# Performance work log

Hardware: AMD Instinct MI355X
Metric: run time of the kernel (lower is better)

The kernel has to match this reference:

```python
import jax, jax.numpy as jnp
import numpy as np

N, IN_FEAT, OUT_FEAT, H = 4096, 256, 256, 8
D = OUT_FEAT // H  # per-head dim = 32
ADJ_DENSITY = 0.05


def setup_inputs() -> dict:
    key = jax.random.key(0)
    kx, kw, kb, ka, kadj = jax.random.split(key, 5)
    x = jax.random.normal(kx, (N, IN_FEAT), dtype=jnp.float32)
    # eqx.nn.Linear params: weight [out, in], bias [out]
    W = jax.random.normal(kw, (OUT_FEAT, IN_FEAT), dtype=jnp.float32) * (1.0 / np.sqrt(IN_FEAT))
    b = jax.random.normal(kb, (OUT_FEAT,), dtype=jnp.float32) * 0.01
    a = jax.random.normal(ka, (H, 2 * D), dtype=jnp.float32)
    adj_matrix = jax.random.bernoulli(kadj, ADJ_DENSITY, (N, N)).astype(jnp.float32)
    return {"x": x, "W": W, "b": b, "a": a, "adj_matrix": adj_matrix}


def reference(x, W, b, a, adj_matrix):
    num_nodes = x.shape[0]
    num_heads = a.shape[0]
    half = a.shape[1] // 2
    # projection: [N, H*D] -> [N, H, D]
    node_feats = (x @ W.T + b).reshape(num_nodes, num_heads, half)
    # per-head additive attention halves -> [N, H]
    logit_parent = (node_feats * a[None, :, :half]).sum(axis=-1)
    logit_child = (node_feats * a[None, :, half:]).sum(axis=-1)
    # [N, N, H] dense logits via broadcast-add
    attn_logits = logit_parent[:, None, :] + logit_child[None, :, :]
    attn_logits = jax.nn.leaky_relu(attn_logits, 0.2)
    # NOTE: faithful to source — masked entries set to 0.0 (not -inf)
    attn_logits = jnp.where(jnp.abs(adj_matrix)[..., None] != 0.0, attn_logits, 0.0)
    attn_probs = jax.nn.softmax(attn_logits, axis=1)
    out = jnp.einsum('ijh,jhc->ihc', attn_probs, node_feats)
    return out.reshape(num_nodes, -1)
```

## Files before the change

kernel.cpp:

```cpp
#include <hip/hip_runtime.h>

#define NN    4096
#define OF    256
#define NH    8
#define MAXNZ 384

typedef __attribute__((ext_vector_type(8))) short short8;
typedef __attribute__((ext_vector_type(4))) float f32x4;

__device__ __forceinline__ float bf2f(unsigned int u) {
    union { unsigned int i; float f; } v; v.i = u << 16; return v.f;
}
__device__ __forceinline__ unsigned short f2bf(float f) {
    union { float f; unsigned int i; } v; v.f = f;
    unsigned int x = v.i;
    return (unsigned short)((x + 0x7fffu + ((x >> 16) & 1u)) >> 16);
}
__device__ __forceinline__ unsigned int pk2bf(float a, float b) {
    return (unsigned int)f2bf(a) | ((unsigned int)f2bf(b) << 16);
}

__global__ __launch_bounds__(256) void k_pre(
    const float* __restrict__ adjf, const float* __restrict__ Wf,
    int* __restrict__ flag, unsigned short* __restrict__ Wbh,
    unsigned short* __restrict__ Wbl, float* __restrict__ zbase)
{
    __shared__ int viol;
    int t = threadIdx.x;
    int gid = blockIdx.x * 256 + t;
    if (t == 0) viol = 0;
    __syncthreads();
    int bad = 0;
    for (int k = t; k < NN; k += 256) {
        float v = adjf[k];
        if (!(v == 0.0f || v == 1.0f)) bad = 1;
    }
    if (bad) atomicAdd(&viol, 1);
    __syncthreads();
    int f = viol > 0;
    if (t == 0) *flag = f;

    zbase[gid] = 0.f;
    if (gid < 256) zbase[65536 + gid] = 0.f;
    if (!f) {
        float v = Wf[gid];
        unsigned short h = f2bf(v);
        Wbh[gid] = h; Wbl[gid] = f2bf(v - bf2f(h));
    }
}

__global__ __launch_bounds__(256) void k_proj(
    const void* __restrict__ xraw, const void* __restrict__ Wraw,
    const void* __restrict__ braw, const void* __restrict__ araw,
    const int* __restrict__ flag,
    const unsigned short* __restrict__ Wbh, const unsigned short* __restrict__ Wbl,
    unsigned short* __restrict__ nfb, float* __restrict__ lp,
    float* __restrict__ lc, float* __restrict__ Stot)
{
    __shared__ unsigned short xh[16][264], xl[16][264];

    int f = *flag;
    int t = threadIdx.x;
    int wave = t >> 6;
    int lane = t & 63;
    int pid = blockIdx.x;

    int tid  = pid * 4 + wave;
    int mt = tid >> 4, nt = tid & 15;
    int lr = lane & 15;
    int kq = (lane >> 4) * 8;

    if (!f) {
        const float* xsrc = (const float*)xraw + (size_t)mt * 4096;
        #pragma unroll
        for (int q = 0; q < 16; q++) {
            int e = t + 256*q;
            float v = xsrc[e];
            unsigned short h = f2bf(v);
            xh[e >> 8][e & 255] = h;
            xl[e >> 8][e & 255] = f2bf(v - bf2f(h));
        }
        __syncthreads();
    }

    size_t wo = (size_t)(nt*16 + lr)*OF + kq;
    f32x4 acc = {0.f, 0.f, 0.f, 0.f};
    if (f) {
        const short8* xp = reinterpret_cast<const short8*>(
            (const unsigned short*)xraw + (size_t)(mt*16 + lr)*OF + kq);
        const short8* wp = reinterpret_cast<const short8*>(
            (const unsigned short*)Wraw + wo);
        #pragma unroll
        for (int kk = 0; kk < OF/32; kk++)
            acc = __builtin_amdgcn_mfma_f32_16x16x32_bf16(xp[kk*4], wp[kk*4], acc, 0, 0, 0);
    } else {
        const short8* wh = reinterpret_cast<const short8*>(Wbh + wo);
        const short8* wl = reinterpret_cast<const short8*>(Wbl + wo);
        #pragma unroll
        for (int kk = 0; kk < OF/32; kk++) {
            short8 ah = *reinterpret_cast<const short8*>(&xh[lr][kk*32 + kq]);
            short8 al = *reinterpret_cast<const short8*>(&xl[lr][kk*32 + kq]);
            short8 bh = wh[kk*4], bl = wl[kk*4];
            acc = __builtin_amdgcn_mfma_f32_16x16x32_bf16(ah, bh, acc, 0, 0, 0);
            acc = __builtin_amdgcn_mfma_f32_16x16x32_bf16(ah, bl, acc, 0, 0, 0);
            acc = __builtin_amdgcn_mfma_f32_16x16x32_bf16(al, bh, acc, 0, 0, 0);
        }
    }

    int col  = nt*16 + lr;
    int row0 = mt*16 + (lane >> 4) * 4;
    int h = col >> 5, cc = col & 31;
    float bias, apar, achd;
    if (f) {
        bias = bf2f((unsigned int)((const unsigned short*)braw)[col]);
        apar = bf2f((unsigned int)((const unsigned short*)araw)[h*64 + cc]);
        achd = bf2f((unsigned int)((const unsigned short*)araw)[h*64 + 32 + cc]);
    } else {
        bias = ((const float*)braw)[col];
        apar = ((const float*)araw)[h*64 + cc];
        achd = ((const float*)araw)[h*64 + 32 + cc];
    }
    float st = 0.f, pr[4], cr[4];
    #pragma unroll
    for (int r = 0; r < 4; r++) {
        float v = acc[r] + bias;
        nfb[(size_t)(row0 + r) * OF + col] = f2bf(v);
        st += v;
        pr[r] = v * apar;
        cr[r] = v * achd;
    }
    #pragma unroll
    for (int m = 1; m <= 8; m <<= 1) {
        #pragma unroll
        for (int r = 0; r < 4; r++) {
            pr[r] += __shfl_xor(pr[r], m, 64);
            cr[r] += __shfl_xor(cr[r], m, 64);
        }
    }
    if ((lane & 15) == 0) {
        #pragma unroll
        for (int r = 0; r < 4; r++) {
            atomicAdd(&lp[(row0 + r) * NH + h], pr[r]);
            atomicAdd(&lc[(row0 + r) * NH + h], cr[r]);
        }
    }
    st += __shfl_down(st, 16, 64);
    st += __shfl_down(st, 32, 64);
    if (lane < 16) atomicAdd(&Stot[col], st);
}

__global__ __launch_bounds__(256, 8) void k_attn(
    const int* __restrict__ flag, const float* __restrict__ adjf,
    const float* __restrict__ lp, const float* __restrict__ lc,
    const unsigned short* __restrict__ nfb, const float* __restrict__ Stot,
    void* __restrict__ outv)
{
    __shared__ int   jro[MAXNZ];
    __shared__ float zred[256];
    __shared__ float gred[3][256];
    __shared__ int   wtot[4];

    int i = blockIdx.x;
    int t = threadIdx.x;
    int lane = t & 63, wid = t >> 6;
    int f = *flag;
    int hh = lane >> 3;
    int slot = lane & 7;
    float lph = lp[i*NH + hh];

    unsigned int m16 = 0;
    if (f) {
        const uint4* ap = reinterpret_cast<const uint4*>(
            (const unsigned short*)adjf + (size_t)i * NN + wid * 1024);
        #pragma unroll
        for (int g = 0; g < 2; g++) {
            uint4 v = ap[lane + 64*g];
            unsigned int wd[4] = {v.x, v.y, v.z, v.w};
            #pragma unroll
            for (int u = 0; u < 4; u++) {
                if (wd[u] & 0xffffu) m16 |= 1u << (g*8 + 2*u);
                if (wd[u] >> 16)     m16 |= 1u << (g*8 + 2*u + 1);
            }
        }
    } else {
        const uint4* ap = reinterpret_cast<const uint4*>(
            adjf + (size_t)i * NN + wid * 1024);
        #pragma unroll
        for (int g = 0; g < 4; g++) {
            uint4 v = ap[lane + 64*g];
            if (v.x) m16 |= 1u << (g*4);
            if (v.y) m16 |= 1u << (g*4 + 1);
            if (v.z) m16 |= 1u << (g*4 + 2);
            if (v.w) m16 |= 1u << (g*4 + 3);
        }
    }

    int pc = __popc(m16);
    int pref = pc;
    #pragma unroll
    for (int off = 1; off < 64; off <<= 1) {
        int u = __shfl_up(pref, off, 64);
        if (lane >= off) pref += u;
    }
    if (lane == 63) wtot[wid] = pref;
    __syncthreads();
    int w0 = wtot[0], w1 = wtot[1], w2 = wtot[2], w3 = wtot[3];
    int n = min(w0 + w1 + w2 + w3, MAXNZ);
    int base = (wid > 0 ? w0 : 0) + (wid > 1 ? w1 : 0) + (wid > 2 ? w2 : 0);
    int pos = base + pref - pc;
    unsigned int mm = m16;
    int jb = wid * 1024;
    while (mm && pos < MAXNZ) {
        int q = __builtin_ctz(mm);
        mm &= mm - 1;
        int j = f ? (jb + lane*8 + ((q >> 3) << 9) + (q & 7))
                  : (jb + lane*4 + ((q >> 2) << 8) + (q & 3));
        jro[pos++] = j * OF;
    }
    __syncthreads();

    int c4 = lane * 4;
    float a0 = 0.f, a1 = 0.f, a2 = 0.f, a3 = 0.f;
    float zp = 0.f;
    int k = wid;
    for (; k + 28 < n; k += 32) {
        int jm = jro[k + 4*slot];
        float s = lph + lc[(jm >> 5) + hh];
        s = fmaxf(s, 0.2f * s);
        float wv = __expf(fminf(s, 70.f)) - 1.f;
        zp += wv;

        int jj[8]; uint2 d[8];
        #pragma unroll
        for (int u = 0; u < 8; u++) {
            jj[u] = __builtin_amdgcn_readfirstlane(jro[k + 4*u]);
            d[u] = *reinterpret_cast<const uint2*>(nfb + jj[u] + c4);
        }
        #pragma unroll
        for (int u = 0; u < 8; u++) {
            float w = __shfl(wv, (lane & ~7) | u, 64);
            a0 += w * bf2f(d[u].x & 0xffffu);
            a1 += w * bf2f(d[u].x >> 16);
            a2 += w * bf2f(d[u].y & 0xffffu);
            a3 += w * bf2f(d[u].y >> 16);
        }
    }
    for (; k < n; k += 4) {
        int j = __builtin_amdgcn_readfirstlane(jro[k]);
        float lcv = lc[(j >> 5) + hh];
        uint2 d = *reinterpret_cast<const uint2*>(nfb + j + c4);
        float s = lph + lcv;
        s = fmaxf(s, 0.2f * s);
        float w = __expf(fminf(s, 70.f)) - 1.f;
        if (slot == 0) zp += w;
        a0 += w * bf2f(d.x & 0xffffu);
        a1 += w * bf2f(d.x >> 16);
        a2 += w * bf2f(d.y & 0xffffu);
        a3 += w * bf2f(d.y >> 16);
    }
    zp += __shfl_xor(zp, 1, 64);
    zp += __shfl_xor(zp, 2, 64);
    zp += __shfl_xor(zp, 4, 64);
    zred[t] = zp;
    if (wid) {
        gred[wid-1][c4]   = a0; gred[wid-1][c4+1] = a1;
        gred[wid-1][c4+2] = a2; gred[wid-1][c4+3] = a3;
    }
    __syncthreads();

    if (wid == 0) {
        float z = zred[hh*8] + zred[64 + hh*8] + zred[128 + hh*8] + zred[192 + hh*8];
        float iz = 1.0f / (4096.0f + z);
        a0 += gred[0][c4]   + gred[1][c4]   + gred[2][c4];
        a1 += gred[0][c4+1] + gred[1][c4+1] + gred[2][c4+1];
        a2 += gred[0][c4+2] + gred[1][c4+2] + gred[2][c4+2];
        a3 += gred[0][c4+3] + gred[1][c4+3] + gred[2][c4+3];
        float4 stv = *reinterpret_cast<const float4*>(Stot + c4);
        float o0 = (stv.x + a0) * iz;
        float o1 = (stv.y + a1) * iz;
        float o2 = (stv.z + a2) * iz;
        float o3 = (stv.w + a3) * iz;
        if (f) {
            uint2 pk; pk.x = pk2bf(o0, o1); pk.y = pk2bf(o2, o3);
            *reinterpret_cast<uint2*>((unsigned short*)outv + (size_t)i*OF + c4) = pk;
        } else {
            float4 o = {o0, o1, o2, o3};
            *reinterpret_cast<float4*>((float*)outv + (size_t)i*OF + c4) = o;
        }
    }
}

extern "C" void kernel_launch(void* const* d_in, const int* in_sizes, int n_in,
                              void* d_out, int out_size, void* d_ws, size_t ws_size,
                              hipStream_t stream) {
    const void* x   = d_in[0];
    const void* W   = d_in[1];
    const void* b   = d_in[2];
    const void* a   = d_in[3];
    const void* adj = d_in[4];

    char* ws = (char*)d_ws;
    const size_t MB = 1024u*1024u, KB = 1024u;
    unsigned short* nfb  = (unsigned short*)(ws);
    float*          lp   = (float*)(ws + 2*MB);
    float*          lc   = (float*)(ws + 2*MB + 128*KB);
    float*          Stot = (float*)(ws + 2*MB + 256*KB);
    int*            flag = (int*)(ws + 2*MB + 257*KB);
    unsigned short* Wbh  = (unsigned short*)(ws + 6*MB);
    unsigned short* Wbl  = (unsigned short*)(ws + 6*MB + 128*KB);

    k_pre  <<<256,  256, 0, stream>>>((const float*)adj, (const float*)W,
                                      flag, Wbh, Wbl, lp);
    k_proj <<<1024, 256, 0, stream>>>(x, W, b, a, flag, Wbh, Wbl,
                                      nfb, lp, lc, Stot);
    k_attn <<<NN,   256, 0, stream>>>(flag, (const float*)adj, lp, lc,
                                      nfb, Stot, d_out);
}
```

Before: 156.6 us.

## Replace sparse gather attention with dense MFMA over transposed node features

The attention kernel no longer compacts nonzero adjacency entries and gathers rows. Each block now takes 16 rows and sweeps all 4096 columns densely. It builds masked exp weights in bf16 and multiplies them with transposed node features using MFMA. The projection kernel writes node features transposed, stores lc head-major and folds log2e into the logits so exp2 can be used. This removes the serial compaction and the irregular gathers, but it does dense work over an adjacency that is about 5% full and rounds the weights to bf16.

```diff
diff --git a/kernel.cpp b/kernel.cpp
--- a/kernel.cpp
+++ b/kernel.cpp
@@ -3,7 +3,6 @@
 #define NN    4096
 #define OF    256
 #define NH    8
-#define MAXNZ 384
 
 typedef __attribute__((ext_vector_type(8))) short short8;
 typedef __attribute__((ext_vector_type(4))) float f32x4;
@@ -18,6 +17,9 @@
 }
 __device__ __forceinline__ unsigned int pk2bf(float a, float b) {
     return (unsigned int)f2bf(a) | ((unsigned int)f2bf(b) << 16);
+}
+__device__ __forceinline__ float asf(unsigned int u) {
+    union { unsigned int i; float f; } v; v.i = u; return v.f;
 }
 
 __global__ __launch_bounds__(256) void k_pre(
@@ -54,7 +56,7 @@
     const void* __restrict__ braw, const void* __restrict__ araw,
     const int* __restrict__ flag,
     const unsigned short* __restrict__ Wbh, const unsigned short* __restrict__ Wbl,
-    unsigned short* __restrict__ nfb, float* __restrict__ lp,
+    unsigned short* __restrict__ nfT, float* __restrict__ lp,
     float* __restrict__ lc, float* __restrict__ Stot)
 {
     __shared__ unsigned short xh[16][264], xl[16][264];
@@ -110,6 +112,7 @@
     int col  = nt*16 + lr;
     int row0 = mt*16 + (lane >> 4) * 4;
     int h = col >> 5, cc = col & 31;
+    const float LOG2E = 1.4426950408889634f;
     float bias, apar, achd;
     if (f) {
         bias = bf2f((unsigned int)((const unsigned short*)braw)[col]);
@@ -120,14 +123,23 @@
         apar = ((const float*)araw)[h*64 + cc];
         achd = ((const float*)araw)[h*64 + 32 + cc];
     }
+    apar *= LOG2E; achd *= LOG2E;
+
+    float vv[4];
+    #pragma unroll
+    for (int r = 0; r < 4; r++) vv[r] = acc[r] + bias;
+
+    uint2 pkv;
+    pkv.x = pk2bf(vv[0], vv[1]);
+    pkv.y = pk2bf(vv[2], vv[3]);
+    *reinterpret_cast<uint2*>(nfT + (size_t)col*NN + row0) = pkv;
+
     float st = 0.f, pr[4], cr[4];
     #pragma unroll
     for (int r = 0; r < 4; r++) {
-        float v = acc[r] + bias;
-        nfb[(size_t)(row0 + r) * OF + col] = f2bf(v);
-        st += v;
-        pr[r] = v * apar;
-        cr[r] = v * achd;
+        st += vv[r];
+        pr[r] = vv[r] * apar;
+        cr[r] = vv[r] * achd;
     }
     #pragma unroll
     for (int m = 1; m <= 8; m <<= 1) {
@@ -141,7 +153,7 @@
         #pragma unroll
         for (int r = 0; r < 4; r++) {
             atomicAdd(&lp[(row0 + r) * NH + h], pr[r]);
-            atomicAdd(&lc[(row0 + r) * NH + h], cr[r]);
+            atomicAdd(&lc[(size_t)h * NN + row0 + r], cr[r]);
         }
     }
     st += __shfl_down(st, 16, 64);
@@ -149,143 +161,96 @@
     if (lane < 16) atomicAdd(&Stot[col], st);
 }
 
-__global__ __launch_bounds__(256, 8) void k_attn(
+__global__ __launch_bounds__(512) void k_attn(
     const int* __restrict__ flag, const float* __restrict__ adjf,
     const float* __restrict__ lp, const float* __restrict__ lc,
-    const unsigned short* __restrict__ nfb, const float* __restrict__ Stot,
+    const unsigned short* __restrict__ nfT, const float* __restrict__ Stot,
     void* __restrict__ outv)
 {
-    __shared__ int   jro[MAXNZ];
-    __shared__ float zred[256];
-    __shared__ float gred[3][256];
-    __shared__ int   wtot[4];
-
-    int i = blockIdx.x;
+    __shared__ float zsh[8][16];
+
+    int i0 = blockIdx.x * 16;
     int t = threadIdx.x;
-    int lane = t & 63, wid = t >> 6;
+    int w = t >> 6;
+    int lane = t & 63;
+    int r = lane & 15;
+    int q = lane >> 4;
     int f = *flag;
-    int hh = lane >> 3;
-    int slot = lane & 7;
-    float lph = lp[i*NH + hh];
-
-    unsigned int m16 = 0;
-    if (f) {
-        const uint4* ap = reinterpret_cast<const uint4*>(
-            (const unsigned short*)adjf + (size_t)i * NN + wid * 1024);
-        #pragma unroll
-        for (int g = 0; g < 2; g++) {
-            uint4 v = ap[lane + 64*g];
-            unsigned int wd[4] = {v.x, v.y, v.z, v.w};
+
+    float lpr = lp[(i0 + r) * NH + w];
+    const float* lcr = lc + (size_t)w * NN;
+    const unsigned short* b0p = nfT + (size_t)(w*32      + r) * NN;
+    const unsigned short* b1p = nfT + (size_t)(w*32 + 16 + r) * NN;
+
+    f32x4 acc0 = {0.f,0.f,0.f,0.f}, acc1 = {0.f,0.f,0.f,0.f};
+    float zacc = 0.f;
+
+    for (int j0 = 0; j0 < NN; j0 += 32) {
+        int jq = j0 + q*8;
+        short8 B0 = *reinterpret_cast<const short8*>(b0p + jq);
+        short8 B1 = *reinterpret_cast<const short8*>(b1p + jq);
+        float4 lca = *reinterpret_cast<const float4*>(lcr + jq);
+        float4 lcb = *reinterpret_cast<const float4*>(lcr + jq + 4);
+        float lv[8] = {lca.x, lca.y, lca.z, lca.w, lcb.x, lcb.y, lcb.z, lcb.w};
+        float mk[8];
+        if (f) {
+            uint4 av = *reinterpret_cast<const uint4*>(
+                (const unsigned short*)adjf + (size_t)(i0 + r) * NN + jq);
+            unsigned int wd[4] = {av.x, av.y, av.z, av.w};
             #pragma unroll
             for (int u = 0; u < 4; u++) {
-                if (wd[u] & 0xffffu) m16 |= 1u << (g*8 + 2*u);
-                if (wd[u] >> 16)     m16 |= 1u << (g*8 + 2*u + 1);
+                mk[2*u]   = bf2f(wd[u] & 0xffffu);
+                mk[2*u+1] = bf2f(wd[u] >> 16);
             }
-        }
-    } else {
-        const uint4* ap = reinterpret_cast<const uint4*>(
-            adjf + (size_t)i * NN + wid * 1024);
-        #pragma unroll
-        for (int g = 0; g < 4; g++) {
-            uint4 v = ap[lane + 64*g];
-            if (v.x) m16 |= 1u << (g*4);
-            if (v.y) m16 |= 1u << (g*4 + 1);
-            if (v.z) m16 |= 1u << (g*4 + 2);
-            if (v.w) m16 |= 1u << (g*4 + 3);
-        }
-    }
-
-    int pc = __popc(m16);
-    int pref = pc;
-    #pragma unroll
-    for (int off = 1; off < 64; off <<= 1) {
-        int u = __shfl_up(pref, off, 64);
-        if (lane >= off) pref += u;
-    }
-    if (lane == 63) wtot[wid] = pref;
+        } else {
+            float4 a0 = *reinterpret_cast<const float4*>(
+                adjf + (size_t)(i0 + r) * NN + jq);
+            float4 a1 = *reinterpret_cast<const float4*>(
+                adjf + (size_t)(i0 + r) * NN + jq + 4);
+            mk[0]=a0.x; mk[1]=a0.y; mk[2]=a0.z; mk[3]=a0.w;
+            mk[4]=a1.x; mk[5]=a1.y; mk[6]=a1.z; mk[7]=a1.w;
+        }
+        float wv[8];
+        #pragma unroll
+        for (int e = 0; e < 8; e++) {
+            float s = lpr + lv[e];
+            s = fmaxf(s, 0.2f * s);
+            s = fminf(s, 101.0f);
+            wv[e] = (exp2f(s) - 1.0f) * mk[e];
+        }
+        union { unsigned int u[4]; short8 s8; } A;
+        #pragma unroll
+        for (int p = 0; p < 4; p++) {
+            unsigned int pk;
+            asm("v_cvt_pk_bf16_f32 %0, %1, %2" : "=v"(pk)
+                : "v"(wv[2*p]), "v"(wv[2*p+1]));
+            A.u[p] = pk;
+            zacc += asf(pk << 16) + asf(pk & 0xffff0000u);
+        }
+        acc0 = __builtin_amdgcn_mfma_f32_16x16x32_bf16(A.s8, B0, acc0, 0, 0, 0);
+        acc1 = __builtin_amdgcn_mfma_f32_16x16x32_bf16(A.s8, B1, acc1, 0, 0, 0);
+    }
+
+    zacc += __shfl_xor(zacc, 16, 64);
+    zacc += __shfl_xor(zacc, 32, 64);
+    if (lane < 16) zsh[w][lane] = zacc;
     __syncthreads();
-    int w0 = wtot[0], w1 = wtot[1], w2 = wtot[2], w3 = wtot[3];
-    int n = min(w0 + w1 + w2 + w3, MAXNZ);
-    int base = (wid > 0 ? w0 : 0) + (wid > 1 ? w1 : 0) + (wid > 2 ? w2 : 0);
-    int pos = base + pref - pc;
-    unsigned int mm = m16;
-    int jb = wid * 1024;
-    while (mm && pos < MAXNZ) {
-        int q = __builtin_ctz(mm);
-        mm &= mm - 1;
-        int j = f ? (jb + lane*8 + ((q >> 3) << 9) + (q & 7))
-                  : (jb + lane*4 + ((q >> 2) << 8) + (q & 3));
-        jro[pos++] = j * OF;
-    }
-    __syncthreads();
-
-    int c4 = lane * 4;
-    float a0 = 0.f, a1 = 0.f, a2 = 0.f, a3 = 0.f;
-    float zp = 0.f;
-    int k = wid;
-    for (; k + 28 < n; k += 32) {
-        int jm = jro[k + 4*slot];
-        float s = lph + lc[(jm >> 5) + hh];
-        s = fmaxf(s, 0.2f * s);
-        float wv = __expf(fminf(s, 70.f)) - 1.f;
-        zp += wv;
-
-        int jj[8]; uint2 d[8];
-        #pragma unroll
-        for (int u = 0; u < 8; u++) {
-            jj[u] = __builtin_amdgcn_readfirstlane(jro[k + 4*u]);
-            d[u] = *reinterpret_cast<const uint2*>(nfb + jj[u] + c4);
-        }
-        #pragma unroll
-        for (int u = 0; u < 8; u++) {
-            float w = __shfl(wv, (lane & ~7) | u, 64);
-            a0 += w * bf2f(d[u].x & 0xffffu);
-            a1 += w * bf2f(d[u].x >> 16);
-            a2 += w * bf2f(d[u].y & 0xffffu);
-            a3 += w * bf2f(d[u].y >> 16);
-        }
-    }
-    for (; k < n; k += 4) {
-        int j = __builtin_amdgcn_readfirstlane(jro[k]);
-        float lcv = lc[(j >> 5) + hh];
-        uint2 d = *reinterpret_cast<const uint2*>(nfb + j + c4);
-        float s = lph + lcv;
-        s = fmaxf(s, 0.2f * s);
-        float w = __expf(fminf(s, 70.f)) - 1.f;
-        if (slot == 0) zp += w;
-        a0 += w * bf2f(d.x & 0xffffu);
-        a1 += w * bf2f(d.x >> 16);
-        a2 += w * bf2f(d.y & 0xffffu);
-        a3 += w * bf2f(d.y >> 16);
-    }
-    zp += __shfl_xor(zp, 1, 64);
-    zp += __shfl_xor(zp, 2, 64);
-    zp += __shfl_xor(zp, 4, 64);
-    zred[t] = zp;
-    if (wid) {
-        gred[wid-1][c4]   = a0; gred[wid-1][c4+1] = a1;
-        gred[wid-1][c4+2] = a2; gred[wid-1][c4+3] = a3;
-    }
-    __syncthreads();
-
-    if (wid == 0) {
-        float z = zred[hh*8] + zred[64 + hh*8] + zred[128 + hh*8] + zred[192 + hh*8];
-        float iz = 1.0f / (4096.0f + z);
-        a0 += gred[0][c4]   + gred[1][c4]   + gred[2][c4];
-        a1 += gred[0][c4+1] + gred[1][c4+1] + gred[2][c4+1];
-        a2 += gred[0][c4+2] + gred[1][c4+2] + gred[2][c4+2];
-        a3 += gred[0][c4+3] + gred[1][c4+3] + gred[2][c4+3];
-        float4 stv = *reinterpret_cast<const float4*>(Stot + c4);
-        float o0 = (stv.x + a0) * iz;
-        float o1 = (stv.y + a1) * iz;
-        float o2 = (stv.z + a2) * iz;
-        float o3 = (stv.w + a3) * iz;
+
+    f32x4 z4 = *reinterpret_cast<f32x4*>(&zsh[w][q*4]);
+    int c0 = w*32 + r, c1 = c0 + 16;
+    float st0 = Stot[c0], st1 = Stot[c1];
+    #pragma unroll
+    for (int reg = 0; reg < 4; reg++) {
+        float iz = 1.0f / (4096.0f + z4[reg]);
+        float o0 = (st0 + acc0[reg]) * iz;
+        float o1 = (st1 + acc1[reg]) * iz;
+        int row = i0 + 4*q + reg;
         if (f) {
-            uint2 pk; pk.x = pk2bf(o0, o1); pk.y = pk2bf(o2, o3);
-            *reinterpret_cast<uint2*>((unsigned short*)outv + (size_t)i*OF + c4) = pk;
+            ((unsigned short*)outv)[(size_t)row*OF + c0] = f2bf(o0);
+            ((unsigned short*)outv)[(size_t)row*OF + c1] = f2bf(o1);
         } else {
-            float4 o = {o0, o1, o2, o3};
-            *reinterpret_cast<float4*>((float*)outv + (size_t)i*OF + c4) = o;
+            ((float*)outv)[(size_t)row*OF + c0] = o0;
+            ((float*)outv)[(size_t)row*OF + c1] = o1;
         }
     }
 }
@@ -301,7 +266,7 @@
 
     char* ws = (char*)d_ws;
     const size_t MB = 1024u*1024u, KB = 1024u;
-    unsigned short* nfb  = (unsigned short*)(ws);
+    unsigned short* nfT  = (unsigned short*)(ws);
     float*          lp   = (float*)(ws + 2*MB);
     float*          lc   = (float*)(ws + 2*MB + 128*KB);
     float*          Stot = (float*)(ws + 2*MB + 256*KB);
@@ -312,7 +277,7 @@
     k_pre  <<<256,  256, 0, stream>>>((const float*)adj, (const float*)W,
                                       flag, Wbh, Wbl, lp);
     k_proj <<<1024, 256, 0, stream>>>(x, W, b, a, flag, Wbh, Wbl,
-                                      nfb, lp, lc, Stot);
-    k_attn <<<NN,   256, 0, stream>>>(flag, (const float*)adj, lp, lc,
-                                      nfb, Stot, d_out);
-}
+                                      nfT, lp, lc, Stot);
+    k_attn <<<256,  512, 0, stream>>>(flag, (const float*)adj, lp, lc,
+                                      nfT, Stot, d_out);
+}
```

New measurement: 244.9 us. 1.56x slower.
